# Performance work log

Hardware: AMD Instinct MI355X
Metric: run time of the kernel (lower is better)

The kernel has to match this reference:

```python
import jax, jax.numpy as jnp
import numpy as np

N = 16384
D_IN = 128
LAYERS = [128, 128, 128, 10]
LATENT = [64, 64]


def _linear_params(key, fan_in, fan_out):
    k1, k2 = jax.random.split(key)
    bound = 1.0 / np.sqrt(fan_in)
    w = jax.random.uniform(k1, (fan_in, fan_out), minval=-bound, maxval=bound, dtype=jnp.float32)
    b = jax.random.uniform(k2, (fan_out,), minval=-bound, maxval=bound, dtype=jnp.float32)
    return w, b


def setup_inputs() -> dict:
    key = jax.random.key(0)
    ks = jax.random.split(key, 8)
    feat_matrix = jax.random.normal(ks[0], (N, D_IN), dtype=jnp.float32)
    gl_w0, gl_b0 = _linear_params(ks[1], LAYERS[0], LATENT[0])
    gnn_w0, gnn_b0 = _linear_params(ks[2], LAYERS[0], LAYERS[1])
    gl_w1, gl_b1 = _linear_params(ks[3], LAYERS[1], LATENT[1])
    gnn_w1, gnn_b1 = _linear_params(ks[4], LAYERS[1], LAYERS[2])
    out_w, out_b = _linear_params(ks[5], LAYERS[2], LAYERS[3])
    return {
        "feat_matrix": feat_matrix,
        "gl_w0": gl_w0, "gl_b0": gl_b0,
        "gl_w1": gl_w1, "gl_b1": gl_b1,
        "gnn_w0": gnn_w0, "gnn_b0": gnn_b0,
        "gnn_w1": gnn_w1, "gnn_b1": gnn_b1,
        "out_w": out_w, "out_b": out_b,
        "temp": jnp.float32(0.1),
        "theta": jnp.float32(0.1),
        "adj_matrix": jnp.zeros((N, N), dtype=jnp.float32),
        "get_item_index": jax.random.randint(ks[6], (1024,), 0, N, dtype=jnp.int32),
        "set_index": jax.random.randint(ks[7], (1024,), 0, N, dtype=jnp.int32),
        "val_index": jax.random.randint(jax.random.fold_in(key, 9), (1024,), 0, N, dtype=jnp.int32),
        "mask_matrix": jnp.zeros((N,), dtype=bool),
    }


def _layer(x, gl_w, gl_b, gnn_w, gnn_b, temp, theta):
    # graph-learning projection
    g = jax.nn.relu(x @ gl_w + gl_b)                     # [N, L]
    # pairwise squared L2 distances (utils.l2_mat)
    sq = jnp.sum(g * g, axis=-1)                         # [N]
    dist = sq[:, None] + sq[None, :] - 2.0 * (g @ g.T)   # [N, N]
    t = 1.0 + temp
    th = 5.0 + theta
    adj = jax.nn.sigmoid(t * (-dist) + th)               # [N, N]
    # diag(rowsum).inverse() @ adj @ gnn(x) == row-normalized message passing
    msg = adj @ (x @ gnn_w + gnn_b)                      # [N, H]
    return msg / jnp.sum(adj, axis=-1, keepdims=True)


def reference(feat_matrix, gl_w0, gl_b0, gl_w1, gl_b1,
              gnn_w0, gnn_b0, gnn_w1, gnn_b1,
              out_w, out_b, temp, theta,
              adj_matrix, get_item_index, set_index, val_index, mask_matrix):
    x = feat_matrix
    x = jax.nn.relu(_layer(x, gl_w0, gl_b0, gnn_w0, gnn_b0, temp, theta))
    x = _layer(x, gl_w1, gl_b1, gnn_w1, gnn_b1, temp, theta)  # last gnn layer: no relu
    x = x @ out_w + out_b
    return jax.nn.softmax(x, axis=-1)
```

## Files before the change

kernel.cpp:

```cpp
#include <hip/hip_runtime.h>

#define NN 16384
#define DL 64
#define HD 128
#define BM 256
#define BN 64
#define JS 8
#define JCH (NN / JS)

typedef _Float16 v8h __attribute__((ext_vector_type(8)));
typedef float v16f __attribute__((ext_vector_type(16)));
typedef unsigned short ushort_t;
typedef unsigned int uint32;

__device__ __forceinline__ float bf2f(ushort_t v) {
  return __uint_as_float(((uint32)v) << 16);
}
__device__ __forceinline__ ushort_t f2bf(float f) {
  uint32 u = __float_as_uint(f);
  return (ushort_t)((u + 0x7FFFu + ((u >> 16) & 1u)) >> 16);
}
__device__ __forceinline__ uint32 pack2h(float a, float b) {
  union { _Float16 h; ushort_t s; } ua, ub;
  ua.h = (_Float16)a; ub.h = (_Float16)b;
  return (uint32)ua.s | ((uint32)ub.s << 16);
}
__device__ __forceinline__ void gld16(void* lds, const void* gp) {
  __builtin_amdgcn_global_load_lds(
      (const __attribute__((address_space(1))) uint32*)gp,
      (__attribute__((address_space(3))) uint32*)lds, 16, 0, 0);
}

__global__ void detect_k(const void* __restrict__ feat,
                         const void* __restrict__ temp,
                         const void* __restrict__ theta,
                         float* __restrict__ consts) {
  if (threadIdx.x == 0) {
    const ushort_t* u = (const ushort_t*)feat;
    int sane = 0;
    for (int i = 0; i < 128; ++i) {
      float v = fabsf(bf2f(u[i]));
      if (v > 1e-4f && v < 16.0f) sane++;
    }
    int isbf = (sane >= 100) ? 1 : 0;
    float tv, th;
    if (isbf) {
      tv = bf2f(((const ushort_t*)temp)[0]);
      th = bf2f(((const ushort_t*)theta)[0]);
    } else {
      tv = ((const float*)temp)[0];
      th = ((const float*)theta)[0];
    }
    consts[0] = (float)isbf;
    consts[1] = 1.0f + tv;
    consts[2] = 5.0f + th;
    consts[3] = 2.0f * (1.0f + tv) * 1.44269504088896341f;
  }
}

template <int L0>
__global__ __launch_bounds__(256) void prep_k(
    const void* __restrict__ xb, const float* __restrict__ pmsg,
    const float* __restrict__ pden, const void* __restrict__ glw,
    const void* __restrict__ glb, const void* __restrict__ gnw,
    const void* __restrict__ gnb, const float* __restrict__ cst,
    _Float16* __restrict__ g, _Float16* __restrict__ hT,
    float* __restrict__ crow) {
  __shared__ float xr[4][128];
  const int w = threadIdx.x >> 6, l = threadIdx.x & 63;
  const int row = blockIdx.x * 4 + w;
  const int isbf = (cst[0] != 0.0f);
  float x0, x1;
  if (L0) {
    if (isbf) {
      const ushort_t* p = (const ushort_t*)xb;
      x0 = bf2f(p[row * 128 + 2 * l]);
      x1 = bf2f(p[row * 128 + 2 * l + 1]);
    } else {
      const float* p = (const float*)xb;
      x0 = p[row * 128 + 2 * l];
      x1 = p[row * 128 + 2 * l + 1];
    }
  } else {
    float rd = __builtin_amdgcn_rcpf(fmaxf(pden[row], 1e-10f));
    float m0 = pmsg[(size_t)row * 128 + 2 * l];
    float m1 = pmsg[(size_t)row * 128 + 2 * l + 1];
    x0 = fmaxf(m0 * rd, 0.0f);
    x1 = fmaxf(m1 * rd, 0.0f);
  }
  xr[w][2 * l] = x0;
  xr[w][2 * l + 1] = x1;
  __syncthreads();
  float ag = 0.0f, a0 = 0.0f, a1 = 0.0f;
  float bg, b0, b1;
  if (isbf) {
    const ushort_t* Wg = (const ushort_t*)glw;
    const ushort_t* Wn = (const ushort_t*)gnw;
#pragma unroll 8
    for (int k = 0; k < 128; ++k) {
      float xk = xr[w][k];
      ag = fmaf(xk, bf2f(Wg[k * 64 + l]), ag);
      a0 = fmaf(xk, bf2f(Wn[k * 128 + l]), a0);
      a1 = fmaf(xk, bf2f(Wn[k * 128 + 64 + l]), a1);
    }
    bg = bf2f(((const ushort_t*)glb)[l]);
    b0 = bf2f(((const ushort_t*)gnb)[l]);
    b1 = bf2f(((const ushort_t*)gnb)[64 + l]);
  } else {
    const float* Wg = (const float*)glw;
    const float* Wn = (const float*)gnw;
#pragma unroll 8
    for (int k = 0; k < 128; ++k) {
      float xk = xr[w][k];
      ag = fmaf(xk, Wg[k * 64 + l], ag);
      a0 = fmaf(xk, Wn[k * 128 + l], a0);
      a1 = fmaf(xk, Wn[k * 128 + 64 + l], a1);
    }
    bg = ((const float*)glb)[l];
    b0 = ((const float*)gnb)[l];
    b1 = ((const float*)gnb)[64 + l];
  }
  const float t = cst[1];
  const float th = cst[2];
  float gv = fmaxf(ag + bg, 0.0f);
  _Float16 gq = (_Float16)gv;
  g[(size_t)row * DL + l] = gq;
  float gf = (float)gq;
  float sq = gf * gf;
#pragma unroll
  for (int off = 1; off < 64; off <<= 1) sq += __shfl_xor(sq, off, 64);
  if (l == 0) crow[row] = (0.5f * th - t * sq) * 1.44269504088896341f;
  hT[(size_t)l * NN + row] = (_Float16)(a0 + b0);
  hT[(size_t)(l + 64) * NN + row] = (_Float16)(a1 + b1);
}

__global__ __launch_bounds__(256, 2) void attn_main(
    const _Float16* __restrict__ g, const _Float16* __restrict__ hT,
    const float* __restrict__ crow, const float* __restrict__ cst,
    float* __restrict__ msg, float* __restrict__ den) {
  __shared__ __align__(16) short SM[4096 + 8192];
  _Float16* Gs = (_Float16*)SM;
  _Float16* Hs = (_Float16*)(SM + 4096);

  const int tid = threadIdx.x;
  const int w = tid >> 6;
  const int l = tid & 63;
  const int ln = l & 31;
  const int hb = l >> 5;
  const int iw = blockIdx.x * BM + w * 64;
  const int jb = blockIdx.y * JCH;
  const float s2 = cst[3];

  v8h Bi[2][4];
#pragma unroll
  for (int it = 0; it < 2; ++it)
#pragma unroll
    for (int kf = 0; kf < 4; ++kf)
      Bi[it][kf] =
          *(const v8h*)(g + (size_t)(iw + it * 32 + ln) * DL + kf * 16 + hb * 8);

  const float ci0 = crow[iw + ln];
  const float ci1 = crow[iw + 32 + ln];

  v16f o[4][2];
#pragma unroll
  for (int mp = 0; mp < 4; ++mp)
#pragma unroll
    for (int it = 0; it < 2; ++it)
#pragma unroll
      for (int r = 0; r < 16; ++r) o[mp][it][r] = 0.0f;

  float dp0 = 0.0f, dp1 = 0.0f;

#pragma unroll 1
  for (int itr = 0; itr < JCH / BN; ++itr) {
    const int j0 = jb + itr * BN;
    __syncthreads();
#pragma unroll
    for (int oo = 0; oo < 2; ++oo) {
      int c = oo * 256 + tid;
      int jj = c >> 3, pc = c & 7;
      int kc = pc ^ (jj & 7);
      gld16((char*)Gs + (oo * 256 + w * 64) * 16,
            g + (size_t)(j0 + jj) * DL + kc * 8);
    }
#pragma unroll
    for (int oo = 0; oo < 4; ++oo) {
      int c = oo * 256 + tid;
      int hc = c >> 3, pc = c & 7;
      int jc = pc ^ (hc & 7);
      gld16((char*)Hs + (oo * 256 + w * 64) * 16,
            hT + (size_t)hc * NN + j0 + jc * 8);
    }
    __syncthreads();

#pragma unroll
    for (int jt = 0; jt < 2; ++jt) {
      float cj[16];
#pragma unroll
      for (int q2 = 0; q2 < 4; ++q2) {
        float4 f4 = *(const float4*)(crow + j0 + jt * 32 + q2 * 8 + 4 * hb);
        cj[q2 * 4 + 0] = f4.x;
        cj[q2 * 4 + 1] = f4.y;
        cj[q2 * 4 + 2] = f4.z;
        cj[q2 * 4 + 3] = f4.w;
      }
      v16f sv[2];
#pragma unroll
      for (int r = 0; r < 16; ++r) {
        sv[0][r] = 0.0f;
        sv[1][r] = 0.0f;
      }
#pragma unroll
      for (int kf = 0; kf < 4; ++kf) {
        int row = jt * 32 + ln;
        int kc = kf * 2 + hb;
        v8h a = *(const v8h*)(Gs + row * 64 + ((kc ^ (row & 7)) * 8));
        sv[0] = __builtin_amdgcn_mfma_f32_32x32x16_f16(a, Bi[0][kf], sv[0], 0, 0, 0);
        sv[1] = __builtin_amdgcn_mfma_f32_32x32x16_f16(a, Bi[1][kf], sv[1], 0, 0, 0);
      }
      uint32 Bf[2][2][4];
#pragma unroll
      for (int it = 0; it < 2; ++it) {
        float pv[16];
        float dps = 0.0f;
        float cib = it ? ci1 : ci0;
#pragma unroll
        for (int r = 0; r < 16; ++r) {
          float arg = fmaf(s2, sv[it][r], cib) + cj[r];
          arg = fminf(fmaxf(arg, -60.0f), 60.0f);
          float e = __builtin_amdgcn_exp2f(-arg);
          float adj = 256.0f * __builtin_amdgcn_rcpf(1.0f + e);
          dps += adj;
          pv[r] = adj;
        }
        if (it == 0) dp0 += dps; else dp1 += dps;
#pragma unroll
        for (int kq = 0; kq < 2; ++kq) {
          int q = kq * 8;
          uint32 lo0 = pack2h(pv[q + 0], pv[q + 1]);
          uint32 lo1 = pack2h(pv[q + 2], pv[q + 3]);
          uint32 hi0 = pack2h(pv[q + 4], pv[q + 5]);
          uint32 hi1 = pack2h(pv[q + 6], pv[q + 7]);
          uint32 sl0 = (uint32)__shfl_xor((int)lo0, 32, 64);
          uint32 sl1 = (uint32)__shfl_xor((int)lo1, 32, 64);
          uint32 sh0 = (uint32)__shfl_xor((int)hi0, 32, 64);
          uint32 sh1 = (uint32)__shfl_xor((int)hi1, 32, 64);
          Bf[it][kq][0] = hb ? sh0 : lo0;
          Bf[it][kq][1] = hb ? sh1 : lo1;
          Bf[it][kq][2] = hb ? hi0 : sl0;
          Bf[it][kq][3] = hb ? hi1 : sl1;
        }
      }
#pragma unroll
      for (int kq = 0; kq < 2; ++kq) {
        union { uint32 u[4]; v8h v; } b0, b1;
        b0.u[0] = Bf[0][kq][0]; b0.u[1] = Bf[0][kq][1];
        b0.u[2] = Bf[0][kq][2]; b0.u[3] = Bf[0][kq][3];
        b1.u[0] = Bf[1][kq][0]; b1.u[1] = Bf[1][kq][1];
        b1.u[2] = Bf[1][kq][2]; b1.u[3] = Bf[1][kq][3];
        int kc = (jt * 2 + kq) * 2 + hb;
#pragma unroll
        for (int mp = 0; mp < 4; ++mp) {
          int hc = mp * 32 + ln;
          v8h Ah = *(const v8h*)(Hs + hc * 64 + ((kc ^ (hc & 7)) * 8));
          o[mp][0] = __builtin_amdgcn_mfma_f32_32x32x16_f16(Ah, b0.v, o[mp][0], 0, 0, 0);
          o[mp][1] = __builtin_amdgcn_mfma_f32_32x32x16_f16(Ah, b1.v, o[mp][1], 0, 0, 0);
        }
      }
    }
  }

  dp0 += __shfl_xor(dp0, 32, 64);
  dp1 += __shfl_xor(dp1, 32, 64);
  if (hb == 0) {
    atomicAdd(&den[iw + ln], dp0);
    atomicAdd(&den[iw + 32 + ln], dp1);
  }
  __syncthreads();
  float* Tw = ((float*)SM) + w * (32 * 33);
#pragma unroll
  for (int mp = 0; mp < 4; ++mp)
#pragma unroll
    for (int it = 0; it < 2; ++it) {
#pragma unroll
      for (int r = 0; r < 16; ++r) {
        int hl = (r & 3) + 8 * (r >> 2) + 4 * hb;
        Tw[ln * 33 + hl] = o[mp][it][r];
      }
#pragma unroll
      for (int rr = 0; rr < 16; ++rr) {
        int il = rr * 2 + hb;
        float v = Tw[il * 33 + ln];
        atomicAdd(&msg[(size_t)(iw + it * 32 + il) * HD + mp * 32 + ln], v);
      }
    }
}

__global__ __launch_bounds__(256) void final_k(
    const float* __restrict__ pmsg, const float* __restrict__ pden,
    const void* __restrict__ ow, const void* __restrict__ ob,
    const float* __restrict__ cst, void* __restrict__ out) {
  __shared__ float Ws[1280];
  const int isbf = (cst[0] != 0.0f);
  if (isbf) {
    for (int i = threadIdx.x; i < 1280; i += 256) Ws[i] = bf2f(((const ushort_t*)ow)[i]);
  } else {
    for (int i = threadIdx.x; i < 1280; i += 256) Ws[i] = ((const float*)ow)[i];
  }
  __syncthreads();
  const int l16 = threadIdx.x & 15, grp = threadIdx.x >> 4;
  const int row = blockIdx.x * 16 + grp;
  const float rd = __builtin_amdgcn_rcpf(fmaxf(pden[row], 1e-10f));
  float acc[10];
#pragma unroll
  for (int c = 0; c < 10; ++c) acc[c] = 0.0f;
#pragma unroll
  for (int kk = 0; kk < 8; ++kk) {
    int k = kk * 16 + l16;
    float xv = pmsg[(size_t)row * 128 + k] * rd;
    xv = fminf(fmaxf(xv, -1e6f), 1e6f);
#pragma unroll
    for (int c = 0; c < 10; ++c) acc[c] = fmaf(xv, Ws[k * 10 + c], acc[c]);
  }
  float bias[10];
  if (isbf) {
#pragma unroll
    for (int c = 0; c < 10; ++c) bias[c] = bf2f(((const ushort_t*)ob)[c]);
  } else {
#pragma unroll
    for (int c = 0; c < 10; ++c) bias[c] = ((const float*)ob)[c];
  }
#pragma unroll
  for (int c = 0; c < 10; ++c) {
#pragma unroll
    for (int off = 1; off < 16; off <<= 1) acc[c] += __shfl_xor(acc[c], off, 64);
    acc[c] += bias[c];
  }
  float m = acc[0];
#pragma unroll
  for (int c = 1; c < 10; ++c) m = fmaxf(m, acc[c]);
  float s = 0.0f, e[10];
#pragma unroll
  for (int c = 0; c < 10; ++c) {
    e[c] = __builtin_amdgcn_exp2f((acc[c] - m) * 1.44269504088896341f);
    s += e[c];
  }
  float rs = __builtin_amdgcn_rcpf(s);
  float mine = e[0];
#pragma unroll
  for (int c = 1; c < 10; ++c) mine = (l16 == c) ? e[c] : mine;
  if (l16 < 10) {
    float v = mine * rs;
    if (isbf) ((ushort_t*)out)[(size_t)row * 10 + l16] = f2bf(v);
    else ((float*)out)[(size_t)row * 10 + l16] = v;
  }
}

extern "C" void kernel_launch(void* const* d_in, const int* in_sizes, int n_in,
                              void* d_out, int out_size, void* d_ws,
                              size_t ws_size, hipStream_t stream) {
  const void* feat = d_in[0];
  const void* glw0 = d_in[1];
  const void* glb0 = d_in[2];
  const void* glw1 = d_in[3];
  const void* glb1 = d_in[4];
  const void* gnw0 = d_in[5];
  const void* gnb0 = d_in[6];
  const void* gnw1 = d_in[7];
  const void* gnb1 = d_in[8];
  const void* ow = d_in[9];
  const void* obv = d_in[10];
  const void* temp = d_in[11];
  const void* thet = d_in[12];

  char* ws = (char*)d_ws;
  _Float16* g = (_Float16*)ws;
  _Float16* hT = (_Float16*)(ws + (size_t)(2u << 20));
  float* crow = (float*)(ws + (size_t)(6u << 20));
  float* msg = (float*)(ws + (size_t)(6u << 20) + (1u << 16));
  float* den = (float*)(ws + (size_t)(14u << 20) + (1u << 16));
  float* cst = (float*)(ws + (size_t)(15u << 20));

  dim3 b256(256);
  detect_k<<<dim3(1), dim3(64), 0, stream>>>(feat, temp, thet, cst);
  prep_k<1><<<dim3(NN / 4), b256, 0, stream>>>(feat, nullptr, nullptr, glw0,
                                               glb0, gnw0, gnb0, cst, g, hT,
                                               crow);
  hipMemsetAsync(msg, 0, (size_t)NN * HD * 4, stream);
  hipMemsetAsync(den, 0, (size_t)NN * 4, stream);
  attn_main<<<dim3(NN / BM, JS), b256, 0, stream>>>(g, hT, crow, cst, msg, den);
  prep_k<0><<<dim3(NN / 4), b256, 0, stream>>>(nullptr, msg, den, glw1, glb1,
                                               gnw1, gnb1, cst, g, hT, crow);
  hipMemsetAsync(msg, 0, (size_t)NN * HD * 4, stream);
  hipMemsetAsync(den, 0, (size_t)NN * 4, stream);
  attn_main<<<dim3(NN / BM, JS), b256, 0, stream>>>(g, hT, crow, cst, msg, den);
  final_k<<<dim3(NN / 16), b256, 0, stream>>>(msg, den, ow, obv, cst, d_out);
}
```

Baseline: 1.735 ms.

## Replace atomic accumulation with per-split partial buffers and halve attention row tile

```diff
diff --git a/kernel.cpp b/kernel.cpp
--- a/kernel.cpp
+++ b/kernel.cpp
@@ -3,7 +3,8 @@
 #define NN 16384
 #define DL 64
 #define HD 128
-#define BM 256
+#define BMW 32
+#define BM 128
 #define BN 64
 #define JS 8
 #define JCH (NN / JS)
@@ -35,14 +36,16 @@
                          const void* __restrict__ temp,
                          const void* __restrict__ theta,
                          float* __restrict__ consts) {
-  if (threadIdx.x == 0) {
-    const ushort_t* u = (const ushort_t*)feat;
-    int sane = 0;
-    for (int i = 0; i < 128; ++i) {
-      float v = fabsf(bf2f(u[i]));
-      if (v > 1e-4f && v < 16.0f) sane++;
-    }
-    int isbf = (sane >= 100) ? 1 : 0;
+  const int l = threadIdx.x;
+  const ushort_t* u = (const ushort_t*)feat;
+  float v0 = fabsf(bf2f(u[2 * l]));
+  float v1 = fabsf(bf2f(u[2 * l + 1]));
+  int ok = ((v0 > 1e-4f && v0 < 16.0f) ? 1 : 0) +
+           ((v1 > 1e-4f && v1 < 16.0f) ? 1 : 0);
+#pragma unroll
+  for (int off = 1; off < 64; off <<= 1) ok += __shfl_xor(ok, off, 64);
+  if (l == 0) {
+    int isbf = (ok >= 100) ? 1 : 0;
     float tv, th;
     if (isbf) {
       tv = bf2f(((const ushort_t*)temp)[0]);
@@ -60,8 +63,8 @@
 
 template <int L0>
 __global__ __launch_bounds__(256) void prep_k(
-    const void* __restrict__ xb, const float* __restrict__ pmsg,
-    const float* __restrict__ pden, const void* __restrict__ glw,
+    const void* __restrict__ xb, const float* __restrict__ msgp,
+    const float* __restrict__ denp, const void* __restrict__ glw,
     const void* __restrict__ glb, const void* __restrict__ gnw,
     const void* __restrict__ gnb, const float* __restrict__ cst,
     _Float16* __restrict__ g, _Float16* __restrict__ hT,
@@ -82,9 +85,15 @@
       x1 = p[row * 128 + 2 * l + 1];
     }
   } else {
-    float rd = __builtin_amdgcn_rcpf(fmaxf(pden[row], 1e-10f));
-    float m0 = pmsg[(size_t)row * 128 + 2 * l];
-    float m1 = pmsg[(size_t)row * 128 + 2 * l + 1];
+    float m0 = 0.0f, m1 = 0.0f, d = 0.0f;
+#pragma unroll
+    for (int js = 0; js < JS; ++js) {
+      const float* mp = msgp + (size_t)js * NN * HD + (size_t)row * HD;
+      m0 += mp[2 * l];
+      m1 += mp[2 * l + 1];
+      d += denp[js * NN + row];
+    }
+    float rd = __builtin_amdgcn_rcpf(fmaxf(d, 1e-10f));
     x0 = fmaxf(m0 * rd, 0.0f);
     x1 = fmaxf(m1 * rd, 0.0f);
   }
@@ -137,7 +146,7 @@
 __global__ __launch_bounds__(256, 2) void attn_main(
     const _Float16* __restrict__ g, const _Float16* __restrict__ hT,
     const float* __restrict__ crow, const float* __restrict__ cst,
-    float* __restrict__ msg, float* __restrict__ den) {
+    float* __restrict__ msgp, float* __restrict__ denp) {
   __shared__ __align__(16) short SM[4096 + 8192];
   _Float16* Gs = (_Float16*)SM;
   _Float16* Hs = (_Float16*)(SM + 4096);
@@ -147,30 +156,24 @@
   const int l = tid & 63;
   const int ln = l & 31;
   const int hb = l >> 5;
-  const int iw = blockIdx.x * BM + w * 64;
+  const int iw = blockIdx.x * BM + w * BMW;
   const int jb = blockIdx.y * JCH;
   const float s2 = cst[3];
 
-  v8h Bi[2][4];
-#pragma unroll
-  for (int it = 0; it < 2; ++it)
-#pragma unroll
-    for (int kf = 0; kf < 4; ++kf)
-      Bi[it][kf] =
-          *(const v8h*)(g + (size_t)(iw + it * 32 + ln) * DL + kf * 16 + hb * 8);
-
-  const float ci0 = crow[iw + ln];
-  const float ci1 = crow[iw + 32 + ln];
-
-  v16f o[4][2];
+  v8h Bi[4];
+#pragma unroll
+  for (int kf = 0; kf < 4; ++kf)
+    Bi[kf] = *(const v8h*)(g + (size_t)(iw + ln) * DL + kf * 16 + hb * 8);
+
+  const float ci = crow[iw + ln];
+
+  v16f o[4];
 #pragma unroll
   for (int mp = 0; mp < 4; ++mp)
 #pragma unroll
-    for (int it = 0; it < 2; ++it)
-#pragma unroll
-      for (int r = 0; r < 16; ++r) o[mp][it][r] = 0.0f;
-
-  float dp0 = 0.0f, dp1 = 0.0f;
+    for (int r = 0; r < 16; ++r) o[mp][r] = 0.0f;
+
+  float dp = 0.0f;
 
 #pragma unroll 1
   for (int itr = 0; itr < JCH / BN; ++itr) {
@@ -205,100 +208,77 @@
         cj[q2 * 4 + 2] = f4.z;
         cj[q2 * 4 + 3] = f4.w;
       }
-      v16f sv[2];
-#pragma unroll
-      for (int r = 0; r < 16; ++r) {
-        sv[0][r] = 0.0f;
-        sv[1][r] = 0.0f;
-      }
+      v16f sv;
+#pragma unroll
+      for (int r = 0; r < 16; ++r) sv[r] = 0.0f;
 #pragma unroll
       for (int kf = 0; kf < 4; ++kf) {
         int row = jt * 32 + ln;
         int kc = kf * 2 + hb;
         v8h a = *(const v8h*)(Gs + row * 64 + ((kc ^ (row & 7)) * 8));
-        sv[0] = __builtin_amdgcn_mfma_f32_32x32x16_f16(a, Bi[0][kf], sv[0], 0, 0, 0);
-        sv[1] = __builtin_amdgcn_mfma_f32_32x32x16_f16(a, Bi[1][kf], sv[1], 0, 0, 0);
+        sv = __builtin_amdgcn_mfma_f32_32x32x16_f16(a, Bi[kf], sv, 0, 0, 0);
       }
-      uint32 Bf[2][2][4];
-#pragma unroll
-      for (int it = 0; it < 2; ++it) {
-        float pv[16];
-        float dps = 0.0f;
-        float cib = it ? ci1 : ci0;
-#pragma unroll
-        for (int r = 0; r < 16; ++r) {
-          float arg = fmaf(s2, sv[it][r], cib) + cj[r];
-          arg = fminf(fmaxf(arg, -60.0f), 60.0f);
-          float e = __builtin_amdgcn_exp2f(-arg);
-          float adj = 256.0f * __builtin_amdgcn_rcpf(1.0f + e);
-          dps += adj;
-          pv[r] = adj;
-        }
-        if (it == 0) dp0 += dps; else dp1 += dps;
-#pragma unroll
-        for (int kq = 0; kq < 2; ++kq) {
-          int q = kq * 8;
-          uint32 lo0 = pack2h(pv[q + 0], pv[q + 1]);
-          uint32 lo1 = pack2h(pv[q + 2], pv[q + 3]);
-          uint32 hi0 = pack2h(pv[q + 4], pv[q + 5]);
-          uint32 hi1 = pack2h(pv[q + 6], pv[q + 7]);
-          uint32 sl0 = (uint32)__shfl_xor((int)lo0, 32, 64);
-          uint32 sl1 = (uint32)__shfl_xor((int)lo1, 32, 64);
-          uint32 sh0 = (uint32)__shfl_xor((int)hi0, 32, 64);
-          uint32 sh1 = (uint32)__shfl_xor((int)hi1, 32, 64);
-          Bf[it][kq][0] = hb ? sh0 : lo0;
-          Bf[it][kq][1] = hb ? sh1 : lo1;
-          Bf[it][kq][2] = hb ? hi0 : sl0;
-          Bf[it][kq][3] = hb ? hi1 : sl1;
-        }
+      float pv[16];
+      float dps = 0.0f;
+#pragma unroll
+      for (int r = 0; r < 16; ++r) {
+        float arg = fmaf(s2, sv[r], ci) + cj[r];
+        arg = fminf(fmaxf(arg, -60.0f), 60.0f);
+        float e = __builtin_amdgcn_exp2f(-arg);
+        float adj = 256.0f * __builtin_amdgcn_rcpf(1.0f + e);
+        dps += adj;
+        pv[r] = adj;
       }
+      dp += dps;
 #pragma unroll
       for (int kq = 0; kq < 2; ++kq) {
-        union { uint32 u[4]; v8h v; } b0, b1;
-        b0.u[0] = Bf[0][kq][0]; b0.u[1] = Bf[0][kq][1];
-        b0.u[2] = Bf[0][kq][2]; b0.u[3] = Bf[0][kq][3];
-        b1.u[0] = Bf[1][kq][0]; b1.u[1] = Bf[1][kq][1];
-        b1.u[2] = Bf[1][kq][2]; b1.u[3] = Bf[1][kq][3];
+        int q = kq * 8;
+        uint32 lo0 = pack2h(pv[q + 0], pv[q + 1]);
+        uint32 lo1 = pack2h(pv[q + 2], pv[q + 3]);
+        uint32 hi0 = pack2h(pv[q + 4], pv[q + 5]);
+        uint32 hi1 = pack2h(pv[q + 6], pv[q + 7]);
+        uint32 sl0 = (uint32)__shfl_xor((int)lo0, 32, 64);
+        uint32 sl1 = (uint32)__shfl_xor((int)lo1, 32, 64);
+        uint32 sh0 = (uint32)__shfl_xor((int)hi0, 32, 64);
+        uint32 sh1 = (uint32)__shfl_xor((int)hi1, 32, 64);
+        union { uint32 u[4]; v8h v; } b;
+        b.u[0] = hb ? sh0 : lo0;
+        b.u[1] = hb ? sh1 : lo1;
+        b.u[2] = hb ? hi0 : sl0;
+        b.u[3] = hb ? hi1 : sl1;
         int kc = (jt * 2 + kq) * 2 + hb;
 #pragma unroll
         for (int mp = 0; mp < 4; ++mp) {
           int hc = mp * 32 + ln;
           v8h Ah = *(const v8h*)(Hs + hc * 64 + ((kc ^ (hc & 7)) * 8));
-          o[mp][0] = __builtin_amdgcn_mfma_f32_32x32x16_f16(Ah, b0.v, o[mp][0], 0, 0, 0);
-          o[mp][1] = __builtin_amdgcn_mfma_f32_32x32x16_f16(Ah, b1.v, o[mp][1], 0, 0, 0);
+          o[mp] = __builtin_amdgcn_mfma_f32_32x32x16_f16(Ah, b.v, o[mp], 0, 0, 0);
         }
       }
     }
   }
 
-  dp0 += __shfl_xor(dp0, 32, 64);
-  dp1 += __shfl_xor(dp1, 32, 64);
-  if (hb == 0) {
-    atomicAdd(&den[iw + ln], dp0);
-    atomicAdd(&den[iw + 32 + ln], dp1);
-  }
+  dp += __shfl_xor(dp, 32, 64);
+  if (hb == 0) denp[blockIdx.y * NN + iw + ln] = dp;
   __syncthreads();
   float* Tw = ((float*)SM) + w * (32 * 33);
-#pragma unroll
-  for (int mp = 0; mp < 4; ++mp)
-#pragma unroll
-    for (int it = 0; it < 2; ++it) {
-#pragma unroll
-      for (int r = 0; r < 16; ++r) {
-        int hl = (r & 3) + 8 * (r >> 2) + 4 * hb;
-        Tw[ln * 33 + hl] = o[mp][it][r];
-      }
-#pragma unroll
-      for (int rr = 0; rr < 16; ++rr) {
-        int il = rr * 2 + hb;
-        float v = Tw[il * 33 + ln];
-        atomicAdd(&msg[(size_t)(iw + it * 32 + il) * HD + mp * 32 + ln], v);
-      }
-    }
+  float* mout = msgp + (size_t)blockIdx.y * NN * HD;
+#pragma unroll
+  for (int mp = 0; mp < 4; ++mp) {
+#pragma unroll
+    for (int r = 0; r < 16; ++r) {
+      int hl = (r & 3) + 8 * (r >> 2) + 4 * hb;
+      Tw[ln * 33 + hl] = o[mp][r];
+    }
+#pragma unroll
+    for (int rr = 0; rr < 16; ++rr) {
+      int il = rr * 2 + hb;
+      mout[(size_t)(iw + il) * HD + mp * 32 + ln] = Tw[il * 33 + ln];
+    }
+  }
 }
 
 __global__ __launch_bounds__(256) void final_k(
-    const float* __restrict__ pmsg, const float* __restrict__ pden,
+    const float* __restrict__ msgp, const float* __restrict__ denp,
     const void* __restrict__ ow, const void* __restrict__ ob,
     const float* __restrict__ cst, void* __restrict__ out) {
   __shared__ float Ws[1280];
@@ -311,14 +291,21 @@
   __syncthreads();
   const int l16 = threadIdx.x & 15, grp = threadIdx.x >> 4;
   const int row = blockIdx.x * 16 + grp;
-  const float rd = __builtin_amdgcn_rcpf(fmaxf(pden[row], 1e-10f));
+  float d = 0.0f;
+#pragma unroll
+  for (int js = 0; js < JS; ++js) d += denp[js * NN + row];
+  const float rd = __builtin_amdgcn_rcpf(fmaxf(d, 1e-10f));
   float acc[10];
 #pragma unroll
   for (int c = 0; c < 10; ++c) acc[c] = 0.0f;
 #pragma unroll
   for (int kk = 0; kk < 8; ++kk) {
     int k = kk * 16 + l16;
-    float xv = pmsg[(size_t)row * 128 + k] * rd;
+    float m = 0.0f;
+#pragma unroll
+    for (int js = 0; js < JS; ++js)
+      m += msgp[(size_t)js * NN * HD + (size_t)row * HD + k];
+    float xv = m * rd;
     xv = fminf(fmaxf(xv, -1e6f), 1e6f);
 #pragma unroll
     for (int c = 0; c < 10; ++c) acc[c] = fmaf(xv, Ws[k * 10 + c], acc[c]);
@@ -378,22 +365,20 @@
   _Float16* g = (_Float16*)ws;
   _Float16* hT = (_Float16*)(ws + (size_t)(2u << 20));
   float* crow = (float*)(ws + (size_t)(6u << 20));
-  float* msg = (float*)(ws + (size_t)(6u << 20) + (1u << 16));
-  float* den = (float*)(ws + (size_t)(14u << 20) + (1u << 16));
-  float* cst = (float*)(ws + (size_t)(15u << 20));
+  float* cst = (float*)(ws + (size_t)(6u << 20) + (1u << 16));
+  float* msgp = (float*)(ws + (size_t)(7u << 20));
+  float* denp = (float*)(ws + (size_t)(71u << 20));
 
   dim3 b256(256);
   detect_k<<<dim3(1), dim3(64), 0, stream>>>(feat, temp, thet, cst);
   prep_k<1><<<dim3(NN / 4), b256, 0, stream>>>(feat, nullptr, nullptr, glw0,
                                                glb0, gnw0, gnb0, cst, g, hT,
                                                crow);
-  hipMemsetAsync(msg, 0, (size_t)NN * HD * 4, stream);
-  hipMemsetAsync(den, 0, (size_t)NN * 4, stream);
-  attn_main<<<dim3(NN / BM, JS), b256, 0, stream>>>(g, hT, crow, cst, msg, den);
-  prep_k<0><<<dim3(NN / 4), b256, 0, stream>>>(nullptr, msg, den, glw1, glb1,
+  attn_main<<<dim3(NN / BM, JS), b256, 0, stream>>>(g, hT, crow, cst, msgp,
+                                                    denp);
+  prep_k<0><<<dim3(NN / 4), b256, 0, stream>>>(nullptr, msgp, denp, glw1, glb1,
                                                gnw1, gnb1, cst, g, hT, crow);
-  hipMemsetAsync(msg, 0, (size_t)NN * HD * 4, stream);
-  hipMemsetAsync(den, 0, (size_t)NN * 4, stream);
-  attn_main<<<dim3(NN / BM, JS), b256, 0, stream>>>(g, hT, crow, cst, msg, den);
-  final_k<<<dim3(NN / 16), b256, 0, stream>>>(msg, den, ow, obv, cst, d_out);
-}
+  attn_main<<<dim3(NN / BM, JS), b256, 0, stream>>>(g, hT, crow, cst, msgp,
+                                                    denp);
+  final_k<<<dim3(NN / 16), b256, 0, stream>>>(msgp, denp, ow, obv, cst, d_out);
+}
```

Result: faster. 1.675 ms (-3.5%).
